# Kernel optimization log

Hardware: AMD Instinct MI355X
Metric: run time of the kernel (lower is better)

The kernel has to match this reference:

```python
import jax, jax.numpy as jnp
import numpy as np

N_NODES = 50000
EMB = 256
HEADS = 2
N_BASE_EDGES = 100000


def setup_inputs() -> dict:
    key = jax.random.key(0)
    ks = jax.random.split(key, 12)
    x = jax.random.normal(ks[0], (N_NODES, EMB), dtype=jnp.float32)
    # bipartite edges: sources in left half, targets in right half -> no self-loops
    src = jax.random.randint(ks[1], (N_BASE_EDGES,), 0, N_NODES // 2)
    dst = jax.random.randint(ks[2], (N_BASE_EDGES,), N_NODES // 2, N_NODES)
    edge_index = jnp.stack([src, dst]).astype(jnp.int64)
    hd = EMB // HEADS
    s = 0.02
    params = {
        "Wkqv": jax.random.normal(ks[3], (EMB, 3 * EMB), dtype=jnp.float32) * s,
        "bkqv": jnp.zeros((3 * EMB,), dtype=jnp.float32),
        "W1": jax.random.normal(ks[4], (2 * hd, hd), dtype=jnp.float32) * s,
        "b1": jnp.zeros((hd,), dtype=jnp.float32),
        "W2": jax.random.normal(ks[5], (hd, 1), dtype=jnp.float32) * s,
        "b2": jnp.zeros((1,), dtype=jnp.float32),
        "Wout": jax.random.normal(ks[6], (EMB, EMB), dtype=jnp.float32) * s,
        "bout": jnp.zeros((EMB,), dtype=jnp.float32),
    }
    return {"x": x, "edge_index": edge_index, **params}


def reference(x, edge_index, Wkqv, bkqv, W1, b1, W2, b2, Wout, bout):
    N, emb = x.shape
    H = HEADS
    hd = emb // H
    # MetaGNNNoEdgeAttr.forward preprocessing: make undirected + self loops.
    # Input is bipartite (no self-loops), so remove_self_loops is a no-op.
    ei = jnp.concatenate([edge_index, edge_index[::-1]], axis=1)
    loops = jnp.arange(N, dtype=edge_index.dtype)
    src = jnp.concatenate([ei[0], loops])  # j (message source)
    dst = jnp.concatenate([ei[1], loops])  # i (message target / softmax index)

    # single GNN layer (n_layers=1)
    kqv = x @ Wkqv + bkqv  # [N, 3*emb]
    q = kqv[dst, :emb].reshape(-1, H, hd)                                  # [E,H,hd]
    k = kqv[src, emb:2 * emb].reshape(-1, H, hd) / jnp.sqrt(jnp.float32(hd))
    v = kqv[src, 2 * emb:].reshape(-1, H, hd)

    h = jax.nn.relu(jnp.concatenate([k, q], axis=-1) @ W1 + b1)  # [E,H,hd]
    a = (h @ W2 + b2).squeeze(-1)                                # [E,H]

    # segment softmax over destination nodes (every node has a self-loop)
    m = jax.ops.segment_max(a, dst, num_segments=N)              # [N,H]
    ex = jnp.exp(a - m[dst])
    s = jax.ops.segment_sum(ex, dst, num_segments=N)             # [N,H]
    alpha = ex / (s[dst] + 1e-16)                                # [E,H]

    msg = (alpha[..., None] * v).reshape(-1, emb) @ Wout + bout  # [E,emb]
    out = jax.ops.segment_sum(msg, dst, num_segments=N)          # [N,emb]
    return jax.nn.relu(out) + x
```

## Files before the change

kernel.cpp:

```cpp
#include <hip/hip_runtime.h>
#include <hip/hip_bf16.h>

#define EMB 256

typedef __bf16 bf16_t;
typedef __attribute__((ext_vector_type(8))) __bf16 bf16x8;
typedef __attribute__((ext_vector_type(4))) __bf16 bf16x4;
typedef __attribute__((ext_vector_type(4))) float floatx4;

__device__ __forceinline__ int eidx(const int* __restrict__ p, int is64, long long k){
  return is64 ? p[2*k] : p[(int)k];
}
__device__ __forceinline__ void async_load16(const void* g, void* l){
  __builtin_amdgcn_global_load_lds(
      (const __attribute__((address_space(1))) unsigned int*)g,
      (__attribute__((address_space(3))) unsigned int*)l,
      16, 0, 0);
}
__device__ __forceinline__ float4 cvt4(bf16x4 v){
  return make_float4((float)v.x, (float)v.y, (float)v.z, (float)v.w);
}
__device__ __forceinline__ int detect64(const int* __restrict__ ei){
  return ((ei[1] | ei[3] | ei[5] | ei[7]) == 0) ? 1 : 0;
}

__global__ void cvt_x_kernel(const float* __restrict__ x, bf16_t* __restrict__ xb, int n4){
  int t = blockIdx.x*blockDim.x + threadIdx.x;
  if (t >= n4) return;
  const float4 v = *(const float4*)(x + (size_t)t*4);
  bf16x4 o = { (bf16_t)v.x, (bf16_t)v.y, (bf16_t)v.z, (bf16_t)v.w };
  *(bf16x4*)(xb + (size_t)t*4) = o;
}

__global__ void prep_weights(const float* __restrict__ Wkqv, const float* __restrict__ bkqv,
                             const float* __restrict__ W1,
                             bf16_t* __restrict__ WcombT, float* __restrict__ bcomb){
  int n = blockIdx.x * blockDim.x + threadIdx.x;
  int c = blockIdx.y;
  if (n >= 768) return;
  const float rs = rsqrtf(128.0f);
  bool isBias = (c == 256);
  const float* arow = isBias ? bkqv : (Wkqv + (size_t)c*768);
  float val;
  if (n < 256){
    int h = n >> 7, d = n & 127;
    float s = 0.f;
    for (int t = 0; t < 128; ++t)
      s = fmaf(arow[h*128 + t], W1[(size_t)(128 + t)*128 + d], s);
    val = s;
  } else {
    int r = n - 256;
    int h = r >> 8, t8 = r & 255;
    int g = t8 >> 3, half = (t8 >> 2) & 1, dd = t8 & 3;
    int d = g*4 + dd;
    if (half == 0){
      float s = 0.f;
      for (int t = 0; t < 128; ++t)
        s = fmaf(arow[256 + h*128 + t], W1[(size_t)t*128 + d], s);
      val = s * rs;
    } else {
      val = arow[512 + h*128 + d];
    }
  }
  if (isBias) bcomb[n] = val;
  else        WcombT[(size_t)n*256 + c] = (bf16_t)val;
}

__global__ void prep_wout(const float* __restrict__ W, bf16_t* __restrict__ Wt){
  int t = blockIdx.x*blockDim.x + threadIdx.x;
  int n = t & 255, c = t >> 8;
  Wt[(size_t)n*256 + c] = (bf16_t)W[(size_t)c*256 + n];
}

__global__ void deg_kernel(const int* __restrict__ ei,
                           int* __restrict__ deg, int E0, int Nn){
  int t = blockIdx.x*blockDim.x + threadIdx.x;
  if (t >= 2*E0) return;
  int is64 = detect64(ei);
  int i = (t < E0) ? eidx(ei,is64,(long long)E0+t) : eidx(ei,is64,t-E0);
  i = min(max(i,0), Nn-1);
  atomicAdd(deg + i, 1);
}

__global__ __launch_bounds__(1024) void scan1_kernel(const int* __restrict__ deg,
                                                     int* __restrict__ off,
                                                     int* __restrict__ bsum, int N){
  __shared__ int wsum[16];
  int tid = threadIdx.x, lane = tid & 63, w = tid >> 6;
  int i = blockIdx.x*1024 + tid;
  int v = (i < N) ? (deg[i] + 1) : 0;
  int incl = v;
  #pragma unroll
  for (int o = 1; o < 64; o <<= 1){
    int t = __shfl_up(incl, o, 64);
    if (lane >= o) incl += t;
  }
  if (lane == 63) wsum[w] = incl;
  __syncthreads();
  if (w == 0 && lane < 16){
    int sv = wsum[lane];
    #pragma unroll
    for (int o = 1; o < 16; o <<= 1){
      int t = __shfl_up(sv, o, 64);
      if (lane >= o) sv += t;
    }
    wsum[lane] = sv;
  }
  __syncthreads();
  int wpref = (w == 0) ? 0 : wsum[w-1];
  if (i < N) off[i] = wpref + incl - v;
  if (tid == 1023) bsum[blockIdx.x] = wpref + incl;
}

__global__ __launch_bounds__(1024) void scan2_kernel(int* __restrict__ bsum,
                                                     int* __restrict__ off, int nb, int N){
  __shared__ int wsum[16];
  int tid = threadIdx.x, lane = tid & 63, w = tid >> 6;
  int v = (tid < nb) ? bsum[tid] : 0;
  int incl = v;
  #pragma unroll
  for (int o = 1; o < 64; o <<= 1){
    int t = __shfl_up(incl, o, 64);
    if (lane >= o) incl += t;
  }
  if (lane == 63) wsum[w] = incl;
  __syncthreads();
  if (w == 0 && lane < 16){
    int sv = wsum[lane];
    #pragma unroll
    for (int o = 1; o < 16; o <<= 1){
      int t = __shfl_up(sv, o, 64);
      if (lane >= o) sv += t;
    }
    wsum[lane] = sv;
  }
  __syncthreads();
  int wpref = (w == 0) ? 0 : wsum[w-1];
  if (tid < nb) bsum[tid] = wpref + incl - v;
  if (tid == 1023) off[N] = wpref + incl;
}

__global__ void scan3_kernel(int* __restrict__ off, const int* __restrict__ bsum, int N){
  int i = blockIdx.x*256 + threadIdx.x;
  if (i < N) off[i] += bsum[i >> 10];
}

__global__ void scatter_kernel(const int* __restrict__ ei,
                               const int* __restrict__ off, int* __restrict__ cursor,
                               int* __restrict__ bj, int E0, int Nn){
  int e = blockIdx.x*blockDim.x + threadIdx.x;
  int E = 2*E0 + Nn;
  if (e >= E) return;
  int is64 = detect64(ei);
  int j, i;
  if (e < E0){ j = eidx(ei,is64,e); i = eidx(ei,is64,(long long)E0+e); }
  else if (e < 2*E0){ int t = e - E0; i = eidx(ei,is64,t); j = eidx(ei,is64,(long long)E0+t); }
  else { i = j = e - 2*E0; }
  i = min(max(i,0), Nn-1); j = min(max(j,0), Nn-1);
  int pos = atomicAdd(cursor + i, 1);
  bj[off[i] + pos] = j;
}

__global__ __launch_bounds__(1024, 4) void mfma_gemm256(
    const bf16_t* __restrict__ A, const bf16_t* __restrict__ Bt,
    const float* __restrict__ bias, bf16_t* __restrict__ C,
    int M, int N)
{
  __shared__ bf16_t As[2][256*32];
  __shared__ bf16_t Bs[2][256*32];
  const int tid = threadIdx.x;
  const int wave = tid >> 6, lane = tid & 63;
  const int row16 = lane & 15, quad = lane >> 4;

  const int nn = N >> 8;
  const int bid = blockIdx.x;
  const int strip = bid / (8*nn);
  const int inner = bid % (8*nn);
  const int m0 = (strip*8 + (inner & 7)) * 256;
  const int n0 = (inner >> 3) * 256;
  const int wm  = (wave >> 2) * 64;
  const int wnq = (wave & 3) * 64;

  const int gm0 = min(m0 + wave*16 + row16, M-1);
  const int gn0 = n0 + wave*16 + row16;

  async_load16(A  + (size_t)gm0*256 + quad*8, (char*)As[0] + wave*1024);
  async_load16(Bt + (size_t)gn0*256 + quad*8, (char*)Bs[0] + wave*1024);

  floatx4 acc[4][4];
  #pragma unroll
  for (int a=0;a<4;++a)
    #pragma unroll
    for (int b=0;b<4;++b) acc[a][b] = (floatx4){0.f,0.f,0.f,0.f};

  #pragma unroll
  for (int kt = 0; kt < 8; ++kt){
    const int cur = kt & 1, nxt = cur ^ 1;
    const int k1 = (kt+1)*32;

    __syncthreads();

    if (kt < 7){
      async_load16(A  + (size_t)gm0*256 + k1 + quad*8, (char*)As[nxt] + wave*1024);
      async_load16(Bt + (size_t)gn0*256 + k1 + quad*8, (char*)Bs[nxt] + wave*1024);
    }

    bf16x8 af[4], bfr[4];
    #pragma unroll
    for (int t = 0; t < 4; ++t){
      af[t]  = *(const bf16x8*)((const char*)As[cur] + ((wm>>4)+t)*1024 + lane*16);
      bfr[t] = *(const bf16x8*)((const char*)Bs[cur] + ((wnq>>4)+t)*1024 + lane*16);
    }
    #pragma unroll
    for (int mt=0;mt<4;++mt)
      #pragma unroll
      for (int nt=0;nt<4;++nt)
        acc[mt][nt] = __builtin_amdgcn_mfma_f32_16x16x32_bf16(bfr[nt], af[mt], acc[mt][nt], 0,0,0);
  }

  float4 b4[4];
  #pragma unroll
  for (int nt=0;nt<4;++nt)
    b4[nt] = *(const float4*)(bias + n0 + wnq + nt*16 + quad*4);

  #pragma unroll
  for (int mt=0;mt<4;++mt){
    const int m = m0 + wm + mt*16 + row16;
    if (m >= M) continue;
    #pragma unroll
    for (int nt=0;nt<4;++nt){
      const int nb = n0 + wnq + nt*16 + quad*4;
      bf16x4 o = { (bf16_t)(acc[mt][nt][0] + b4[nt].x),
                   (bf16_t)(acc[mt][nt][1] + b4[nt].y),
                   (bf16_t)(acc[mt][nt][2] + b4[nt].z),
                   (bf16_t)(acc[mt][nt][3] + b4[nt].w) };
      *(bf16x4*)(C + (size_t)m*N + nb) = o;
    }
  }
}

__global__ __launch_bounds__(512, 4) void mfma_gemm_m1(
    const bf16_t* __restrict__ A, const bf16_t* __restrict__ Bt,
    const float* __restrict__ bias, float* __restrict__ C,
    int M, int N,
    const int* __restrict__ deg, const float* __restrict__ xres)
{
  __shared__ bf16_t As[2][128*32];
  __shared__ bf16_t Bs[2][128*32];
  const int tid = threadIdx.x;
  const int wave = tid >> 6, lane = tid & 63;
  const int row16 = lane & 15, quad = lane >> 4;

  const int nn = N >> 7;
  const int bid = blockIdx.x;
  const int strip = bid / (8*nn);
  const int inner = bid % (8*nn);
  const int m0 = (strip*8 + (inner & 7)) * 128;
  const int n0 = (inner >> 3) * 128;
  const int wm  = (wave >> 2) * 64;
  const int wnq = (wave & 3) * 32;

  const int f0 = wave;
  const int gm0 = min(m0 + f0*16 + row16, M-1);
  const int gn0 = n0 + f0*16 + row16;

  async_load16(A  + (size_t)gm0*256 + quad*8, (char*)As[0] + f0*1024);
  async_load16(Bt + (size_t)gn0*256 + quad*8, (char*)Bs[0] + f0*1024);

  floatx4 acc[4][2];
  #pragma unroll
  for (int a=0;a<4;++a)
    #pragma unroll
    for (int b=0;b<2;++b) acc[a][b] = (floatx4){0.f,0.f,0.f,0.f};

  #pragma unroll
  for (int kt = 0; kt < 8; ++kt){
    const int cur = kt & 1, nxt = cur ^ 1;
    const int k1 = (kt+1)*32;

    __syncthreads();

    if (kt < 7){
      async_load16(A  + (size_t)gm0*256 + k1 + quad*8, (char*)As[nxt] + f0*1024);
      async_load16(Bt + (size_t)gn0*256 + k1 + quad*8, (char*)Bs[nxt] + f0*1024);
    }

    bf16x8 af[4], bfr[2];
    #pragma unroll
    for (int t = 0; t < 4; ++t)
      af[t]  = *(const bf16x8*)((const char*)As[cur] + ((wm>>4)+t)*1024 + lane*16);
    #pragma unroll
    for (int u = 0; u < 2; ++u)
      bfr[u] = *(const bf16x8*)((const char*)Bs[cur] + ((wnq>>4)+u)*1024 + lane*16);

    #pragma unroll
    for (int mt=0;mt<4;++mt)
      #pragma unroll
      for (int nt=0;nt<2;++nt)
        acc[mt][nt] = __builtin_amdgcn_mfma_f32_16x16x32_bf16(bfr[nt], af[mt], acc[mt][nt], 0,0,0);
  }

  float4 b4[2];
  #pragma unroll
  for (int nt=0;nt<2;++nt)
    b4[nt] = *(const float4*)(bias + n0 + wnq + nt*16 + quad*4);

  #pragma unroll
  for (int mt=0;mt<4;++mt){
    const int m = m0 + wm + mt*16 + row16;
    if (m >= M) continue;
    const float dg = (float)(deg[m]+1);
    #pragma unroll
    for (int nt=0;nt<2;++nt){
      const int nb = n0 + wnq + nt*16 + quad*4;
      const float4 xr = *(const float4*)(xres + (size_t)m*N + nb);
      float4 o;
      o.x = fmaxf(acc[mt][nt][0] + dg*b4[nt].x, 0.f) + xr.x;
      o.y = fmaxf(acc[mt][nt][1] + dg*b4[nt].y, 0.f) + xr.y;
      o.z = fmaxf(acc[mt][nt][2] + dg*b4[nt].z, 0.f) + xr.z;
      o.w = fmaxf(acc[mt][nt][3] + dg*b4[nt].w, 0.f) + xr.w;
      *(float4*)(C + (size_t)m*N + nb) = o;
    }
  }
}

__device__ __forceinline__ float score4(bf16x8 kvv, float4 qv, float4 b1v, float4 w2v){
  return fmaxf(qv.x+(float)kvv[0]+b1v.x, 0.f)*w2v.x
       + fmaxf(qv.y+(float)kvv[1]+b1v.y, 0.f)*w2v.y
       + fmaxf(qv.z+(float)kvv[2]+b1v.z, 0.f)*w2v.z
       + fmaxf(qv.w+(float)kvv[3]+b1v.w, 0.f)*w2v.w;
}
__device__ __forceinline__ float hredux(float p){
  #pragma unroll
  for (int o = 16; o >= 1; o >>= 1)
    p += __shfl_xor(p, o, 64);
  return p;
}
__global__ __launch_bounds__(256) void fused_attn_kernel(
    const bf16_t* __restrict__ P, const int* __restrict__ bj, const int* __restrict__ off,
    const float* __restrict__ b1, const float* __restrict__ W2, const float* __restrict__ b2,
    bf16_t* __restrict__ aggb, int Nn)
{
  int i = blockIdx.x * (blockDim.x >> 6) + (threadIdx.x >> 6);
  if (i >= Nn) return;
  int lane = threadIdx.x & 63;
  int h = lane >> 5, g = lane & 31, d = g * 4;

  const float4 qv  = cvt4(*(const bf16x4*)(P + (size_t)i*768 + h*128 + d));
  const float4 b1v = *(const float4*)(b1 + d);
  const float4 w2v = *(const float4*)(W2 + d);
  const float b2v  = b2[0];
  const bf16_t* __restrict__ Pkv = P + 256 + h*256 + g*8;

  float m = -3.0e38f, s = 0.f;
  float4 acc = make_float4(0.f,0.f,0.f,0.f);
  const int s0 = off[i], s1 = off[i+1], s1m1 = s1 - 1;

  for (int t = s0; t < s1; t += 4){
    const int cnt = s1 - t;
    const int jA = bj[t];
    const int jB = bj[min(t+1, s1m1)];
    const int jC = bj[min(t+2, s1m1)];
    const int jD = bj[min(t+3, s1m1)];
    const bf16x8 kA = *(const bf16x8*)(Pkv + (size_t)jA*768);
    const bf16x8 kB = *(const bf16x8*)(Pkv + (size_t)jB*768);
    const bf16x8 kC = *(const bf16x8*)(Pkv + (size_t)jC*768);
    const bf16x8 kD = *(const bf16x8*)(Pkv + (size_t)jD*768);
    float pA = hredux(score4(kA, qv, b1v, w2v));
    float pB = hredux(score4(kB, qv, b1v, w2v));
    float pC = hredux(score4(kC, qv, b1v, w2v));
    float pD = hredux(score4(kD, qv, b1v, w2v));
    const float aA = pA + b2v;
    const float aB = (cnt > 1) ? pB + b2v : -3.0e38f;
    const float aC = (cnt > 2) ? pC + b2v : -3.0e38f;
    const float aD = (cnt > 3) ? pD + b2v : -3.0e38f;
    const float amax = fmaxf(fmaxf(aA, aB), fmaxf(aC, aD));
    const float mn = fmaxf(m, amax);
    const float sc = __expf(m - mn);
    const float eA = __expf(aA - mn);
    const float eB = __expf(aB - mn);
    const float eC = __expf(aC - mn);
    const float eD = __expf(aD - mn);
    s = s*sc + ((eA + eB) + (eC + eD));
    acc.x = acc.x*sc + ((eA*(float)kA[4] + eB*(float)kB[4]) + (eC*(float)kC[4] + eD*(float)kD[4]));
    acc.y = acc.y*sc + ((eA*(float)kA[5] + eB*(float)kB[5]) + (eC*(float)kC[5] + eD*(float)kD[5]));
    acc.z = acc.z*sc + ((eA*(float)kA[6] + eB*(float)kB[6]) + (eC*(float)kC[6] + eD*(float)kD[6]));
    acc.w = acc.w*sc + ((eA*(float)kA[7] + eB*(float)kB[7]) + (eC*(float)kC[7] + eD*(float)kD[7]));
    m = mn;
  }
  float inv = 1.f / (s + 1e-16f);
  bf16x4 ob = { (bf16_t)(acc.x*inv), (bf16_t)(acc.y*inv), (bf16_t)(acc.z*inv), (bf16_t)(acc.w*inv) };
  *(bf16x4*)(aggb + (size_t)i*256 + h*128 + d) = ob;
}

extern "C" void kernel_launch(void* const* d_in, const int* in_sizes, int n_in,
                              void* d_out, int out_size, void* d_ws, size_t ws_size,
                              hipStream_t stream)
{
  const float* x     = (const float*)d_in[0];
  const int*   ei    = (const int*)d_in[1];
  const float* Wkqv  = (const float*)d_in[2];
  const float* bkqv  = (const float*)d_in[3];
  const float* W1    = (const float*)d_in[4];
  const float* b1    = (const float*)d_in[5];
  const float* W2    = (const float*)d_in[6];
  const float* b2    = (const float*)d_in[7];
  const float* Wout  = (const float*)d_in[8];
  const float* bout  = (const float*)d_in[9];
  float* out = (float*)d_out;

  const int N  = in_sizes[0] / EMB;
  const int E0 = in_sizes[1] / 2;
  const int E  = 2*E0 + N;

  float* base = (float*)d_ws;
  bf16_t* WcombT = (bf16_t*)base;
  float*  bcomb  = base + 98304;
  bf16_t* WoutT  = (bf16_t*)(base + 98304 + 768);
  bf16_t* xb     = (bf16_t*)(base + 131840);
  bf16_t* Pb     = (bf16_t*)(base + 131840 + 6400000);
  bf16_t* aggb   = (bf16_t*)(Pb + (size_t)N*768);
  int* deg       = (int*)(aggb + (size_t)N*256);
  int* cursor    = deg + N;
  int* flag      = cursor + N;
  int* off       = flag + 1;
  int* bj        = off + (N+1);
  int* bsum      = (int*)aggb;

  hipMemsetAsync(deg, 0, (size_t)2*N*sizeof(int), stream);

  cvt_x_kernel<<<((N*EMB/4)+255)/256,256,0,stream>>>(x, xb, N*EMB/4);
  prep_weights<<<dim3(3,257),256,0,stream>>>(Wkqv, bkqv, W1, WcombT, bcomb);
  prep_wout<<<256,256,0,stream>>>(Wout, WoutT);

  deg_kernel<<<(2*E0+255)/256,256,0,stream>>>(ei, deg, E0, N);
  const int nb = (N + 1023)/1024;
  scan1_kernel<<<nb,1024,0,stream>>>(deg, off, bsum, N);
  scan2_kernel<<<1,1024,0,stream>>>(bsum, off, nb, N);
  scan3_kernel<<<(N+255)/256,256,0,stream>>>(off, bsum, N);
  scatter_kernel<<<(E+255)/256,256,0,stream>>>(ei, off, cursor, bj, E0, N);

  const int nm256 = (((N+255)/256) + 7) & ~7;
  mfma_gemm256<<<nm256*3,1024,0,stream>>>(xb, WcombT, bcomb, Pb, N, 768);
  fused_attn_kernel<<<(N+3)/4,256,0,stream>>>(Pb, bj, off, b1, W2, b2, aggb, N);
  const int nm128 = (((N+127)/128) + 7) & ~7;
  mfma_gemm_m1<<<nm128*2,512,0,stream>>>(aggb, WoutT, bout, out, N, 256, deg, x);
}
```

Before: 290.1 us.

## Overlap CSR graph build on a side stream and widen output GEMM tile

Moves the degree count, prefix scans and edge scatter onto a second non-blocking stream, forked and joined with events, so they run concurrently with input conversion, weight prep and the QKV GEMM. The output projection GEMM now computes all 256 output columns per block (4x4 MFMA tiles per wave), halving the grid and removing the duplicate loads of A rows. This adds stream/event management and more registers and LDS per block, which may reduce occupancy.

```diff
diff --git a/kernel.cpp b/kernel.cpp
--- a/kernel.cpp
+++ b/kernel.cpp
@@ -246,32 +246,29 @@
     const int* __restrict__ deg, const float* __restrict__ xres)
 {
   __shared__ bf16_t As[2][128*32];
-  __shared__ bf16_t Bs[2][128*32];
+  __shared__ bf16_t Bs[2][256*32];
   const int tid = threadIdx.x;
   const int wave = tid >> 6, lane = tid & 63;
   const int row16 = lane & 15, quad = lane >> 4;
 
-  const int nn = N >> 7;
   const int bid = blockIdx.x;
-  const int strip = bid / (8*nn);
-  const int inner = bid % (8*nn);
-  const int m0 = (strip*8 + (inner & 7)) * 128;
-  const int n0 = (inner >> 3) * 128;
+  const int m0 = ((bid/8)*8 + (bid & 7)) * 128;
   const int wm  = (wave >> 2) * 64;
-  const int wnq = (wave & 3) * 32;
-
-  const int f0 = wave;
-  const int gm0 = min(m0 + f0*16 + row16, M-1);
-  const int gn0 = n0 + f0*16 + row16;
-
-  async_load16(A  + (size_t)gm0*256 + quad*8, (char*)As[0] + f0*1024);
-  async_load16(Bt + (size_t)gn0*256 + quad*8, (char*)Bs[0] + f0*1024);
-
-  floatx4 acc[4][2];
+  const int wnq = (wave & 3) * 64;
+
+  const int gm0 = min(m0 + wave*16 + row16, M-1);
+  const int gnA = wave*16 + row16;
+  const int gnB = (wave+8)*16 + row16;
+
+  async_load16(A  + (size_t)gm0*256 + quad*8, (char*)As[0] + wave*1024);
+  async_load16(Bt + (size_t)gnA*256 + quad*8, (char*)Bs[0] + wave*1024);
+  async_load16(Bt + (size_t)gnB*256 + quad*8, (char*)Bs[0] + (wave+8)*1024);
+
+  floatx4 acc[4][4];
   #pragma unroll
   for (int a=0;a<4;++a)
     #pragma unroll
-    for (int b=0;b<2;++b) acc[a][b] = (floatx4){0.f,0.f,0.f,0.f};
+    for (int b=0;b<4;++b) acc[a][b] = (floatx4){0.f,0.f,0.f,0.f};
 
   #pragma unroll
   for (int kt = 0; kt < 8; ++kt){
@@ -281,29 +278,28 @@
     __syncthreads();
 
     if (kt < 7){
-      async_load16(A  + (size_t)gm0*256 + k1 + quad*8, (char*)As[nxt] + f0*1024);
-      async_load16(Bt + (size_t)gn0*256 + k1 + quad*8, (char*)Bs[nxt] + f0*1024);
-    }
-
-    bf16x8 af[4], bfr[2];
-    #pragma unroll
-    for (int t = 0; t < 4; ++t)
+      async_load16(A  + (size_t)gm0*256 + k1 + quad*8, (char*)As[nxt] + wave*1024);
+      async_load16(Bt + (size_t)gnA*256 + k1 + quad*8, (char*)Bs[nxt] + wave*1024);
+      async_load16(Bt + (size_t)gnB*256 + k1 + quad*8, (char*)Bs[nxt] + (wave+8)*1024);
+    }
+
+    bf16x8 af[4], bfr[4];
+    #pragma unroll
+    for (int t = 0; t < 4; ++t){
       af[t]  = *(const bf16x8*)((const char*)As[cur] + ((wm>>4)+t)*1024 + lane*16);
-    #pragma unroll
-    for (int u = 0; u < 2; ++u)
-      bfr[u] = *(const bf16x8*)((const char*)Bs[cur] + ((wnq>>4)+u)*1024 + lane*16);
-
+      bfr[t] = *(const bf16x8*)((const char*)Bs[cur] + ((wnq>>4)+t)*1024 + lane*16);
+    }
     #pragma unroll
     for (int mt=0;mt<4;++mt)
       #pragma unroll
-      for (int nt=0;nt<2;++nt)
+      for (int nt=0;nt<4;++nt)
         acc[mt][nt] = __builtin_amdgcn_mfma_f32_16x16x32_bf16(bfr[nt], af[mt], acc[mt][nt], 0,0,0);
   }
 
-  float4 b4[2];
-  #pragma unroll
-  for (int nt=0;nt<2;++nt)
-    b4[nt] = *(const float4*)(bias + n0 + wnq + nt*16 + quad*4);
+  float4 b4[4];
+  #pragma unroll
+  for (int nt=0;nt<4;++nt)
+    b4[nt] = *(const float4*)(bias + wnq + nt*16 + quad*4);
 
   #pragma unroll
   for (int mt=0;mt<4;++mt){
@@ -311,8 +307,8 @@
     if (m >= M) continue;
     const float dg = (float)(deg[m]+1);
     #pragma unroll
-    for (int nt=0;nt<2;++nt){
-      const int nb = n0 + wnq + nt*16 + quad*4;
+    for (int nt=0;nt<4;++nt){
+      const int nb = wnq + nt*16 + quad*4;
       const float4 xr = *(const float4*)(xres + (size_t)m*N + nb);
       float4 o;
       o.x = fmaxf(acc[mt][nt][0] + dg*b4[nt].x, 0.f) + xr.x;
@@ -427,22 +423,35 @@
   int* bj        = off + (N+1);
   int* bsum      = (int*)aggb;
 
-  hipMemsetAsync(deg, 0, (size_t)2*N*sizeof(int), stream);
+  static hipStream_t s1 = nullptr;
+  static hipEvent_t evFork = nullptr, evJoin = nullptr;
+  if (s1 == nullptr){
+    hipStreamCreateWithFlags(&s1, hipStreamNonBlocking);
+    hipEventCreateWithFlags(&evFork, hipEventDisableTiming);
+    hipEventCreateWithFlags(&evJoin, hipEventDisableTiming);
+  }
+
+  hipEventRecord(evFork, stream);
+  hipStreamWaitEvent(s1, evFork, 0);
+
+  hipMemsetAsync(deg, 0, (size_t)2*N*sizeof(int), s1);
+  deg_kernel<<<(2*E0+255)/256,256,0,s1>>>(ei, deg, E0, N);
+  const int nb = (N + 1023)/1024;
+  scan1_kernel<<<nb,1024,0,s1>>>(deg, off, bsum, N);
+  scan2_kernel<<<1,1024,0,s1>>>(bsum, off, nb, N);
+  scan3_kernel<<<(N+255)/256,256,0,s1>>>(off, bsum, N);
+  scatter_kernel<<<(E+255)/256,256,0,s1>>>(ei, off, cursor, bj, E0, N);
 
   cvt_x_kernel<<<((N*EMB/4)+255)/256,256,0,stream>>>(x, xb, N*EMB/4);
   prep_weights<<<dim3(3,257),256,0,stream>>>(Wkqv, bkqv, W1, WcombT, bcomb);
   prep_wout<<<256,256,0,stream>>>(Wout, WoutT);
-
-  deg_kernel<<<(2*E0+255)/256,256,0,stream>>>(ei, deg, E0, N);
-  const int nb = (N + 1023)/1024;
-  scan1_kernel<<<nb,1024,0,stream>>>(deg, off, bsum, N);
-  scan2_kernel<<<1,1024,0,stream>>>(bsum, off, nb, N);
-  scan3_kernel<<<(N+255)/256,256,0,stream>>>(off, bsum, N);
-  scatter_kernel<<<(E+255)/256,256,0,stream>>>(ei, off, cursor, bj, E0, N);
-
   const int nm256 = (((N+255)/256) + 7) & ~7;
   mfma_gemm256<<<nm256*3,1024,0,stream>>>(xb, WcombT, bcomb, Pb, N, 768);
+
+  hipEventRecord(evJoin, s1);
+  hipStreamWaitEvent(stream, evJoin, 0);
+
   fused_attn_kernel<<<(N+3)/4,256,0,stream>>>(Pb, bj, off, b1, W2, b2, aggb, N);
   const int nm128 = (((N+127)/128) + 7) & ~7;
-  mfma_gemm_m1<<<nm128*2,512,0,stream>>>(aggb, WoutT, bout, out, N, 256, deg, x);
-}
+  mfma_gemm_m1<<<nm128,512,0,stream>>>(aggb, WoutT, bout, out, N, 256, deg, x);
+}
```

After: 314.4 us. 1.08x slower.
